# Kernel optimization log

Measured on AMD Instinct MI355X. Metric: run time of the kernel, lower is better.

Reference implementation:

```python
import jax, jax.numpy as jnp
import numpy as np

B, T, C, H = 8, 2048, 384, 64

def setup_inputs() -> dict:
    key = jax.random.key(0)
    k1, k2, k3, k4 = jax.random.split(key, 4)
    x = jax.random.normal(k1, (B, T, C), dtype=jnp.float32)
    Wq = jax.random.normal(k2, (C, H), dtype=jnp.float32) * (C ** -0.5)
    Wk = jax.random.normal(k3, (C, H), dtype=jnp.float32) * (C ** -0.5)
    Wv = jax.random.normal(k4, (C, H), dtype=jnp.float32) * (C ** -0.5)
    return {"x": x, "Wq": Wq, "Wk": Wk, "Wv": Wv}

def reference(x, Wq, Wk, Wv):
    # x: (B, T, C); projections: (B, T, H)
    Bn, Tn, Cn = x.shape
    q = jnp.einsum('btc,ch->bth', x, Wq)
    k = jnp.einsum('btc,ch->bth', x, Wk)
    v = jnp.einsum('btc,ch->bth', x, Wv)
    # NOTE: source scales by C**-0.5 (embedding dim), not head_size**-0.5
    weights = jnp.einsum('bth,bsh->bts', q, k) * (Cn ** -0.5)  # (B, T, T)
    causal = jnp.tril(jnp.ones((Tn, Tn), dtype=bool))
    weights = jnp.where(causal, weights, -jnp.inf)
    # NOTE: source applies softmax over dim=1 (query/row axis), reproduced faithfully
    weights = jax.nn.softmax(weights, axis=1)
    # dropout omitted (eval-mode reference)
    return jnp.einsum('bts,bsh->bth', weights, v)
```

## Files before the change

### kernel.cpp

```cpp
#include <hip/hip_runtime.h>
#include <hip/hip_bf16.h>
#include <math.h>

#define Bn 8
#define Tn 2048
#define Cn 384
#define Hn 64
#define SCALE 0.051031036307982884f
#define SCALE2 0.07362240熙f_IGNORE
#undef SCALE2
#define SCALE2 0.07362241f

using bf16x8 = __attribute__((ext_vector_type(8))) short;
using f32x4  = __attribute__((ext_vector_type(4))) float;

#define MFMA(a, b, c) __builtin_amdgcn_mfma_f32_16x16x32_bf16((a), (b), (c), 0, 0, 0)

static __device__ __forceinline__ short f2bf(float f) {
  unsigned u = __float_as_uint(f);
  u += 0x7fffu + ((u >> 16) & 1u);
  return (short)(u >> 16);
}
static __device__ __forceinline__ float bf2f(short s) {
  return __uint_as_float(((unsigned)(unsigned short)s) << 16);
}
static __device__ __forceinline__ float fexp2(float x) {
#if __has_builtin(__builtin_amdgcn_exp2f)
  return __builtin_amdgcn_exp2f(x);
#else
  return exp2f(x);
#endif
}

__global__ __launch_bounds__(256) void wconv_kernel(
    const float* __restrict__ Wq, const float* __restrict__ Wk,
    const float* __restrict__ Wv, short* __restrict__ WbT) {
  int idx = blockIdx.x * 256 + threadIdx.x;
  int n = idx / 384, k = idx - n * 384;
  const float* W = (n < 64) ? Wq : (n < 128) ? Wk : Wv;
  WbT[idx] = f2bf(W[k * 64 + (n & 63)]);
}

__global__ __launch_bounds__(256) void proj_kernel(
    const float* __restrict__ x, const short* __restrict__ WbT,
    short* __restrict__ qb, short* __restrict__ kb, short* __restrict__ vT) {
  __shared__ short xs[16][392];
  __shared__ short vtile[64][20];
  const int tid = threadIdx.x;
  const int t0 = blockIdx.x * 16;
  const float* xb = x + (size_t)t0 * Cn;
  #pragma unroll
  for (int i = 0; i < 6; ++i) {
    int j = tid + i * 256;
    int row = j / 96, colv = (j - row * 96) * 4;
    float4 v = *(const float4*)(xb + row * Cn + colv);
    short4 s4; s4.x = f2bf(v.x); s4.y = f2bf(v.y); s4.z = f2bf(v.z); s4.w = f2bf(v.w);
    *(short4*)(&xs[row][colv]) = s4;
  }
  __syncthreads();
  const int w = tid >> 6, l15 = tid & 15, quad = (tid & 63) >> 4;
  f32x4 acc[3] = {};
  for (int ks = 0; ks < 12; ++ks) {
    bf16x8 a = *(const bf16x8*)(&xs[l15][ks * 32 + quad * 8]);
    #pragma unroll
    for (int cf = 0; cf < 3; ++cf) {
      bf16x8 bfr = *(const bf16x8*)(WbT + (size_t)(48 * w + 16 * cf + l15) * Cn + ks * 32 + quad * 8);
      acc[cf] = MFMA(a, bfr, acc[cf]);
    }
  }
  #pragma unroll
  for (int cf = 0; cf < 3; ++cf) {
    int cbase = 48 * w + 16 * cf, c = cbase + l15;
    #pragma unroll
    for (int r = 0; r < 4; ++r) {
      int row = t0 + quad * 4 + r;
      short val = f2bf(acc[cf][r]);
      if (cbase < 64)       qb[(size_t)row * Hn + c] = val;
      else if (cbase < 128) kb[(size_t)row * Hn + (c - 64)] = val;
      else                  vtile[c - 128][quad * 4 + r] = val;
    }
  }
  __syncthreads();
  const int b = t0 >> 11, t0l = t0 & 2047;
  int h = tid >> 2, tseg = (tid & 3) * 4;
  *(short4*)(vT + ((size_t)(b * Hn + h)) * Tn + t0l + tseg) =
      *(const short4*)(&vtile[h][tseg]);
}

__global__ __launch_bounds__(256) void colstats_kernel(
    const short* __restrict__ qb, const short* __restrict__ kb,
    float* __restrict__ pL, short* __restrict__ Eb) {
  const int unit = blockIdx.x;
  const int b = unit >> 7, rem = unit & 127;
  const int j = rem >> 3, u = rem & 7;
  const int lo = (u * 33) >> 3, hi = ((u + 1) * 33) >> 3;
  const int big = 32 - j;
  const int tid = threadIdx.x, w = tid >> 6, l15 = tid & 15, quad = (tid & 63) >> 4;
  const size_t Ebase = (size_t)b * Tn * Tn;
  __shared__ float redl[64][17];

  auto run = [&](const int i, const int k0, const int k1, const int slot) {
    const int s0 = i << 6;
    float l[4] = {0.f, 0.f, 0.f, 0.f};
    const int n = k1 - k0;
    if (n > 0) {
      bf16x8 bk[8];
      #pragma unroll
      for (int nf = 0; nf < 4; ++nf) {
        const size_t krow = (size_t)(b * Tn + s0 + 16 * nf + l15) * Hn;
        bk[2 * nf]     = *(const bf16x8*)(kb + krow + quad * 8);
        bk[2 * nf + 1] = *(const bf16x8*)(kb + krow + 32 + quad * 8);
      }
      auto cload = [&](bf16x8& A0, bf16x8& A1, int k) {
        size_t ar = (size_t)(b * Tn + ((i + k) << 6) + 16 * w + l15) * Hn;
        A0 = *(const bf16x8*)(qb + ar + quad * 8);
        A1 = *(const bf16x8*)(qb + ar + 32 + quad * 8);
      };
      auto ccomp = [&](bf16x8 A0, bf16x8 A1, int k) {
        f32x4 sc[4] = {};
        #pragma unroll
        for (int nf = 0; nf < 4; ++nf) {
          sc[nf] = MFMA(A0, bk[2 * nf], sc[nf]);
          sc[nf] = MFMA(A1, bk[2 * nf + 1], sc[nf]);
        }
        const bool diag = (k == 0);
        const int tb = ((i + k) << 6) + 16 * w + quad * 4;
        #pragma unroll
        for (int nf = 0; nf < 4; ++nf) {
          int s = s0 + 16 * nf + l15;
          #pragma unroll
          for (int r = 0; r < 4; ++r) {
            float v = sc[nf][r] * SCALE2;
            if (diag && (tb + r) < s) v = -INFINITY;
            float ev = fexp2(v);
            l[nf] += ev;
            Eb[Ebase + (size_t)(tb + r) * Tn + s] = f2bf(ev);
          }
        }
      };
      bf16x8 a0A, a1A, a0B, a1B, a0C, a1C;
      cload(a0A, a1A, k0);
      if (n > 1) cload(a0B, a1B, k0 + 1);
      if (n > 2) cload(a0C, a1C, k0 + 2);
      int k = k0;
      while (k + 3 < k1) {
        ccomp(a0A, a1A, k);     cload(a0A, a1A, k + 3);
        ccomp(a0B, a1B, k + 1); if (k + 4 < k1) cload(a0B, a1B, k + 4);
        ccomp(a0C, a1C, k + 2); if (k + 5 < k1) cload(a0C, a1C, k + 5);
        k += 3;
      }
      const int rem2 = k1 - k;
      if (rem2 > 0) ccomp(a0A, a1A, k);
      if (rem2 > 1) ccomp(a0B, a1B, k + 1);
      if (rem2 > 2) ccomp(a0C, a1C, k + 2);
    }
    __syncthreads();
    #pragma unroll
    for (int nf = 0; nf < 4; ++nf) redl[16 * nf + l15][w * 4 + quad] = l[nf];
    __syncthreads();
    if (tid < 64) {
      float ls = 0.f;
      #pragma unroll
      for (int q2 = 0; q2 < 16; ++q2) ls += redl[tid][q2];
      pL[unit * 128 + slot * 64 + tid] = ls;
    }
  };
  run(j, lo, min(hi, big), 0);
  run(31 - j, max(lo, big) - big, hi - big, 1);
}

__global__ __launch_bounds__(256) void vhat_kernel(
    const short* __restrict__ vT, const float* __restrict__ pL,
    short* __restrict__ vS, float* __restrict__ outz) {
  int gid = blockIdx.x * 256 + threadIdx.x;
  size_t base = (size_t)gid * 8;
  int b = (int)(base >> 17), s = (int)(base & 2047);
  int i = s >> 6, c = s & 63;
  int j2 = (i < 16) ? i : 31 - i;
  int slot = (i < 16) ? 0 : 1;
  const float* pp = pL + (size_t)((b * 16 + j2) * 8) * 128 + slot * 64 + c;
  float L0x = 0.f, L0y = 0.f, L0z = 0.f, L0w = 0.f;
  float L1x = 0.f, L1y = 0.f, L1z = 0.f, L1w = 0.f;
  #pragma unroll
  for (int u = 0; u < 8; ++u) {
    float4 p0 = *(const float4*)(pp + u * 128);
    float4 p1 = *(const float4*)(pp + u * 128 + 4);
    L0x += p0.x; L0y += p0.y; L0z += p0.z; L0w += p0.w;
    L1x += p1.x; L1y += p1.y; L1z += p1.z; L1w += p1.w;
  }
  short4 v0 = *(const short4*)(vT + base);
  short4 v1 = *(const short4*)(vT + base + 4);
  short4 r0, r1;
  r0.x = f2bf(bf2f(v0.x) / L0x); r0.y = f2bf(bf2f(v0.y) / L0y);
  r0.z = f2bf(bf2f(v0.z) / L0z); r0.w = f2bf(bf2f(v0.w) / L0w);
  r1.x = f2bf(bf2f(v1.x) / L1x); r1.y = f2bf(bf2f(v1.y) / L1y);
  r1.z = f2bf(bf2f(v1.z) / L1z); r1.w = f2bf(bf2f(v1.w) / L1w);
  *(short4*)(vS + base) = r0;
  *(short4*)(vS + base + 4) = r1;
  float4 z = {0.f, 0.f, 0.f, 0.f};
  *(float4*)(outz + base) = z;
  *(float4*)(outz + base + 4) = z;
}

__global__ __launch_bounds__(256) void outg_kernel(
    const short* __restrict__ Eb, const short* __restrict__ vS,
    float* __restrict__ out) {
  const int unit = blockIdx.x;
  const int b = unit >> 7, rem = unit & 127;
  const int j = rem >> 3, u = rem & 7;
  const int lo = (u * 33) >> 3, hi = ((u + 1) * 33) >> 3;
  const int big = 32 - j;
  const int tid = threadIdx.x, w = tid >> 6, l15 = tid & 15, quad = (tid & 63) >> 4;
  const size_t Bbase = (size_t)b * Hn * Tn;

  auto run = [&](const int tile, const int k0, const int k1) {
    if (k0 >= k1) return;
    const int tbase = (tile << 6) + 16 * w;
    const size_t Abase = (size_t)b * Tn * Tn + (size_t)(tbase + l15) * Tn;
    f32x4 acc[4] = {};
    bf16x8 aA[2], bA[8], aB[2], bB[8];
    auto load = [&](bf16x8 (&A)[2], bf16x8 (&Bf)[8], int ch) {
      const int s0 = ch << 6;
      A[0] = *(const bf16x8*)(Eb + Abase + s0 + quad * 8);
      A[1] = *(const bf16x8*)(Eb + Abase + s0 + 32 + quad * 8);
      #pragma unroll
      for (int nf = 0; nf < 4; ++nf) {
        const size_t br = Bbase + (size_t)(16 * nf + l15) * Tn + s0;
        Bf[2 * nf]     = *(const bf16x8*)(vS + br + quad * 8);
        Bf[2 * nf + 1] = *(const bf16x8*)(vS + br + 32 + quad * 8);
      }
    };
    auto comp = [&](bf16x8 (&A)[2], bf16x8 (&Bf)[8]) {
      #pragma unroll
      for (int nf = 0; nf < 4; ++nf) {
        acc[nf] = MFMA(A[0], Bf[2 * nf], acc[nf]);
        acc[nf] = MFMA(A[1], Bf[2 * nf + 1], acc[nf]);
      }
    };
    load(aA, bA, k0);
    int ch = k0;
    while (ch + 1 < k1) {
      load(aB, bB, ch + 1);
      comp(aA, bA);
      if (ch + 2 < k1) load(aA, bA, ch + 2);
      comp(aB, bB);
      ch += 2;
    }
    if (ch < k1) comp(aA, bA);
    #pragma unroll
    for (int nf = 0; nf < 4; ++nf)
      #pragma unroll
      for (int r = 0; r < 4; ++r)
        atomicAdd(&out[(size_t)(b * Tn + tbase + quad * 4 + r) * Hn + 16 * nf + l15],
                  acc[nf][r]);
  };
  run(31 - j, lo, min(hi, big));
  run(j, max(lo, big) - big, hi - big);
}

extern "C" void kernel_launch(void* const* d_in, const int* in_sizes, int n_in,
                              void* d_out, int out_size, void* d_ws, size_t ws_size,
                              hipStream_t stream) {
  const float* x  = (const float*)d_in[0];
  const float* Wq = (const float*)d_in[1];
  const float* Wk = (const float*)d_in[2];
  const float* Wv = (const float*)d_in[3];
  char* ws = (char*)d_ws;
  short* qb   = (short*)(ws);
  short* kb   = (short*)(ws + 2097152);
  short* vT   = (short*)(ws + 4194304);
  short* vS   = (short*)(ws + 6291456);
  short* WbT  = (short*)(ws + 8388608);
  float* pL   = (float*)(ws + 8536064);
  short* Eb   = (short*)(ws + 16777216);
  float* outp = (float*)d_out;

  hipLaunchKernelGGL(wconv_kernel, dim3(288), dim3(256), 0, stream, Wq, Wk, Wv, WbT);
  hipLaunchKernelGGL(proj_kernel, dim3(Bn * Tn / 16), dim3(256), 0, stream, x, WbT, qb, kb, vT);
  hipLaunchKernelGGL(colstats_kernel, dim3(1024), dim3(256), 0, stream, qb, kb, pL, Eb);
  hipLaunchKernelGGL(vhat_kernel, dim3(512), dim3(256), 0, stream, vT, pL, vS, outp);
  hipLaunchKernelGGL(outg_kernel, dim3(1024), dim3(256), 0, stream, Eb, vS, outp);
}
```

Measured before the change: 144.5 us.

## Recompute exp scores in output kernel instead of materializing bf16 E matrix

Drops the B×T×T bf16 exponentiated score matrix that colstats wrote and outg read back. Instead, outg recomputes QK^T for each 64-wide chunk with MFMA, applies the causal mask and exp2, and stages the bf16 probabilities through swizzled per-wave LDS to reshape them into A-operand layout for the PV MFMA. This removes roughly tens of MB of global writes and reads, at the cost of doing the QK matmul and exp twice and adding an LDS round trip per chunk.

```diff
diff --git a/kernel.cpp b/kernel.cpp
--- a/kernel.cpp
+++ b/kernel.cpp
@@ -6,13 +6,11 @@
 #define Tn 2048
 #define Cn 384
 #define Hn 64
-#define SCALE 0.051031036307982884f
-#define SCALE2 0.07362240熙f_IGNORE
-#undef SCALE2
 #define SCALE2 0.07362241f
 
 using bf16x8 = __attribute__((ext_vector_type(8))) short;
 using f32x4  = __attribute__((ext_vector_type(4))) float;
+using u32x4  = __attribute__((ext_vector_type(4))) unsigned;
 
 #define MFMA(a, b, c) __builtin_amdgcn_mfma_f32_16x16x32_bf16((a), (b), (c), 0, 0, 0)
 
@@ -30,6 +28,9 @@
 #else
   return exp2f(x);
 #endif
+}
+static __device__ __forceinline__ unsigned pack2(float lo, float hi) {
+  return (unsigned)(unsigned short)f2bf(lo) | ((unsigned)(unsigned short)f2bf(hi) << 16);
 }
 
 __global__ __launch_bounds__(256) void wconv_kernel(
@@ -89,14 +90,13 @@
 
 __global__ __launch_bounds__(256) void colstats_kernel(
     const short* __restrict__ qb, const short* __restrict__ kb,
-    float* __restrict__ pL, short* __restrict__ Eb) {
+    float* __restrict__ pL) {
   const int unit = blockIdx.x;
   const int b = unit >> 7, rem = unit & 127;
   const int j = rem >> 3, u = rem & 7;
   const int lo = (u * 33) >> 3, hi = ((u + 1) * 33) >> 3;
   const int big = 32 - j;
   const int tid = threadIdx.x, w = tid >> 6, l15 = tid & 15, quad = (tid & 63) >> 4;
-  const size_t Ebase = (size_t)b * Tn * Tn;
   __shared__ float redl[64][17];
 
   auto run = [&](const int i, const int k0, const int k1, const int slot) {
@@ -132,9 +132,7 @@
           for (int r = 0; r < 4; ++r) {
             float v = sc[nf][r] * SCALE2;
             if (diag && (tb + r) < s) v = -INFINITY;
-            float ev = fexp2(v);
-            l[nf] += ev;
-            Eb[Ebase + (size_t)(tb + r) * Tn + s] = f2bf(ev);
+            l[nf] += fexp2(v);
           }
         }
       };
@@ -203,55 +201,91 @@
 }
 
 __global__ __launch_bounds__(256) void outg_kernel(
-    const short* __restrict__ Eb, const short* __restrict__ vS,
-    float* __restrict__ out) {
+    const short* __restrict__ qb, const short* __restrict__ kb,
+    const short* __restrict__ vS, float* __restrict__ out) {
   const int unit = blockIdx.x;
   const int b = unit >> 7, rem = unit & 127;
   const int j = rem >> 3, u = rem & 7;
   const int lo = (u * 33) >> 3, hi = ((u + 1) * 33) >> 3;
   const int big = 32 - j;
   const int tid = threadIdx.x, w = tid >> 6, l15 = tid & 15, quad = (tid & 63) >> 4;
-  const size_t Bbase = (size_t)b * Hn * Tn;
+  __shared__ unsigned plds_raw[4][512];
+  char* pw = (char*)(&plds_raw[w][0]);
+  const int swz = (l15 & 7) << 4;
+  int wroff[8];
+  #pragma unroll
+  for (int nf = 0; nf < 4; ++nf)
+    #pragma unroll
+    for (int p = 0; p < 2; ++p)
+      wroff[2 * nf + p] = l15 * 128 + ((nf * 32 + quad * 8 + p * 4) ^ swz);
+  const int rd0 = l15 * 128 + ((quad * 16) ^ swz);
+  const int rd1 = l15 * 128 + ((64 + quad * 16) ^ swz);
+  const size_t QKbase = (size_t)b * Tn * Hn;
+  const size_t Vbase  = (size_t)b * Hn * Tn;
 
   auto run = [&](const int tile, const int k0, const int k1) {
     if (k0 >= k1) return;
     const int tbase = (tile << 6) + 16 * w;
-    const size_t Abase = (size_t)b * Tn * Tn + (size_t)(tbase + l15) * Tn;
+    const size_t qrow = QKbase + (size_t)(tbase + l15) * Hn;
+    const bf16x8 qf0 = *(const bf16x8*)(qb + qrow + quad * 8);
+    const bf16x8 qf1 = *(const bf16x8*)(qb + qrow + 32 + quad * 8);
+    const int tg = tbase + l15;
     f32x4 acc[4] = {};
-    bf16x8 aA[2], bA[8], aB[2], bB[8];
-    auto load = [&](bf16x8 (&A)[2], bf16x8 (&Bf)[8], int ch) {
+    bf16x8 kf[8];
+    auto loadK = [&](int ch) {
       const int s0 = ch << 6;
-      A[0] = *(const bf16x8*)(Eb + Abase + s0 + quad * 8);
-      A[1] = *(const bf16x8*)(Eb + Abase + s0 + 32 + quad * 8);
-      #pragma unroll
-      for (int nf = 0; nf < 4; ++nf) {
-        const size_t br = Bbase + (size_t)(16 * nf + l15) * Tn + s0;
-        Bf[2 * nf]     = *(const bf16x8*)(vS + br + quad * 8);
-        Bf[2 * nf + 1] = *(const bf16x8*)(vS + br + 32 + quad * 8);
+      #pragma unroll
+      for (int nf = 0; nf < 4; ++nf) {
+        const size_t kr = QKbase + (size_t)(s0 + 16 * nf + l15) * Hn;
+        kf[2 * nf]     = *(const bf16x8*)(kb + kr + quad * 8);
+        kf[2 * nf + 1] = *(const bf16x8*)(kb + kr + 32 + quad * 8);
       }
     };
-    auto comp = [&](bf16x8 (&A)[2], bf16x8 (&Bf)[8]) {
-      #pragma unroll
-      for (int nf = 0; nf < 4; ++nf) {
-        acc[nf] = MFMA(A[0], Bf[2 * nf], acc[nf]);
-        acc[nf] = MFMA(A[1], Bf[2 * nf + 1], acc[nf]);
-      }
-    };
-    load(aA, bA, k0);
-    int ch = k0;
-    while (ch + 1 < k1) {
-      load(aB, bB, ch + 1);
-      comp(aA, bA);
-      if (ch + 2 < k1) load(aA, bA, ch + 2);
-      comp(aB, bB);
-      ch += 2;
-    }
-    if (ch < k1) comp(aA, bA);
+    loadK(k0);
+    for (int ch = k0; ch < k1; ++ch) {
+      const int s0 = ch << 6;
+      f32x4 sc[4] = {};
+      #pragma unroll
+      for (int nf = 0; nf < 4; ++nf) {
+        sc[nf] = MFMA(kf[2 * nf], qf0, sc[nf]);
+        sc[nf] = MFMA(kf[2 * nf + 1], qf1, sc[nf]);
+      }
+      if (ch + 1 < k1) loadK(ch + 1);
+      bf16x8 vf[8];
+      #pragma unroll
+      for (int nf = 0; nf < 4; ++nf) {
+        const size_t vr = Vbase + (size_t)(16 * nf + l15) * Tn + s0;
+        vf[2 * nf]     = *(const bf16x8*)(vS + vr + quad * 8);
+        vf[2 * nf + 1] = *(const bf16x8*)(vS + vr + 32 + quad * 8);
+      }
+      const bool diag = (ch == tile);
+      #pragma unroll
+      for (int nf = 0; nf < 4; ++nf) {
+        float ev[4];
+        #pragma unroll
+        for (int r = 0; r < 4; ++r) {
+          float v = sc[nf][r] * SCALE2;
+          const int s = s0 + 16 * nf + quad * 4 + r;
+          if (diag && tg < s) v = -INFINITY;
+          ev[r] = fexp2(v);
+        }
+        *(unsigned*)(pw + wroff[2 * nf])     = pack2(ev[0], ev[1]);
+        *(unsigned*)(pw + wroff[2 * nf + 1]) = pack2(ev[2], ev[3]);
+      }
+      __asm__ __volatile__("" ::: "memory");
+      const bf16x8 a0 = __builtin_bit_cast(bf16x8, *(const u32x4*)(pw + rd0));
+      const bf16x8 a1 = __builtin_bit_cast(bf16x8, *(const u32x4*)(pw + rd1));
+      #pragma unroll
+      for (int nf = 0; nf < 4; ++nf) {
+        acc[nf] = MFMA(a0, vf[2 * nf], acc[nf]);
+        acc[nf] = MFMA(a1, vf[2 * nf + 1], acc[nf]);
+      }
+    }
     #pragma unroll
     for (int nf = 0; nf < 4; ++nf)
       #pragma unroll
       for (int r = 0; r < 4; ++r)
-        atomicAdd(&out[(size_t)(b * Tn + tbase + quad * 4 + r) * Hn + 16 * nf + l15],
+        atomicAdd(&out[QKbase + (size_t)(tbase + quad * 4 + r) * Hn + 16 * nf + l15],
                   acc[nf][r]);
   };
   run(31 - j, lo, min(hi, big));
@@ -272,12 +306,11 @@
   short* vS   = (short*)(ws + 6291456);
   short* WbT  = (short*)(ws + 8388608);
   float* pL   = (float*)(ws + 8536064);
-  short* Eb   = (short*)(ws + 16777216);
   float* outp = (float*)d_out;
 
   hipLaunchKernelGGL(wconv_kernel, dim3(288), dim3(256), 0, stream, Wq, Wk, Wv, WbT);
   hipLaunchKernelGGL(proj_kernel, dim3(Bn * Tn / 16), dim3(256), 0, stream, x, WbT, qb, kb, vT);
-  hipLaunchKernelGGL(colstats_kernel, dim3(1024), dim3(256), 0, stream, qb, kb, pL, Eb);
+  hipLaunchKernelGGL(colstats_kernel, dim3(1024), dim3(256), 0, stream, qb, kb, pL);
   hipLaunchKernelGGL(vhat_kernel, dim3(512), dim3(256), 0, stream, vT, pL, vS, outp);
-  hipLaunchKernelGGL(outg_kernel, dim3(1024), dim3(256), 0, stream, Eb, vS, outp);
-}
+  hipLaunchKernelGGL(outg_kernel, dim3(1024), dim3(256), 0, stream, qb, kb, vS, outp);
+}
```

After: 162.5 us. +12.5%, slower.
